# Kernel optimization log

Hardware: AMD Instinct MI355X
Metric: run time of the kernel (lower is better)

## Reference

```python
import jax, jax.numpy as jnp
import numpy as np

EPS = 1e-08
ATOM_CA = 1


def setup_inputs() -> dict:
    key = jax.random.key(0)
    k1, k2 = jax.random.split(key)
    B, N_RES, N_ATOMS = 256, 1024, 37
    pred_coords = jax.random.normal(k1, (B, N_RES, N_ATOMS, 3), dtype=jnp.float32)
    true_coords = jax.random.normal(k2, (B, N_RES, N_ATOMS, 3), dtype=jnp.float32)
    atom_mask = jnp.ones((B, N_RES, N_ATOMS), dtype=jnp.float32)
    return {"pred_coords": pred_coords, "true_coords": true_coords, "atom_mask": atom_mask}


def _kabsch_align(pred, true, mask):
    # pred/true: [B, N, 3], mask: [B, N]
    mask_sum = jnp.sum(mask, axis=1, keepdims=True) + EPS          # [B, 1]
    m = mask[..., None]                                             # [B, N, 1]
    pred_center = jnp.sum(pred * m, axis=1) / mask_sum              # [B, 3]
    true_center = jnp.sum(true * m, axis=1) / mask_sum              # [B, 3]
    pred_c = (pred - pred_center[:, None, :]) * m                   # [B, N, 3]
    true_c = (true - true_center[:, None, :]) * m                   # [B, N, 3]
    H = jnp.einsum('bni,bnj->bij', pred_c, true_c)                  # [B, 3, 3]
    U, s, Vh = jnp.linalg.svd(H)                                    # H = U diag(s) Vh
    V = jnp.swapaxes(Vh, -1, -2)
    Ut = jnp.swapaxes(U, -1, -2)
    det = jnp.linalg.det(jnp.matmul(V, Ut))                         # [B]
    sign = jnp.stack([jnp.ones_like(det), jnp.ones_like(det), det], axis=-1)  # [B, 3]
    S = jnp.eye(3, dtype=pred.dtype) * sign[:, None, :]             # diag(1,1,det)
    R = jnp.matmul(jnp.matmul(V, S), Ut)                            # [B, 3, 3]
    # aligned = (pred - pred_center) @ R^T + true_center
    aligned = jnp.einsum('bnj,bij->bni', pred - pred_center[:, None, :], R)
    return aligned + true_center[:, None, :]


def reference(pred_coords, true_coords, atom_mask):
    pred_ca = pred_coords[:, :, ATOM_CA, :]   # [B, N_res, 3]
    true_ca = true_coords[:, :, ATOM_CA, :]
    ca_mask = atom_mask[:, :, ATOM_CA]        # [B, N_res]
    pred_ca = _kabsch_align(pred_ca, true_ca, ca_mask)
    diff_sq = jnp.sum((pred_ca - true_ca) ** 2, axis=-1)            # [B, N_res]
    rmsd = jnp.sqrt(jnp.sum(diff_sq * ca_mask, axis=1) / (jnp.sum(ca_mask, axis=1) + EPS))
    return jnp.mean(rmsd)
```

## Files before the change

kernel.cpp:

```cpp
#include <hip/hip_runtime.h>
#include <math.h>

#define N_RES 1024
#define N_ATOMS 37
#define ATOM_CA 1
#define NBATCH 256
#define SLICES 2
#define NSUM 18

struct F3 { float x, y, z; };

__global__ __launch_bounds__(256) void rmsd_fused_kernel(
    const float* __restrict__ pred, const float* __restrict__ truec,
    const float* __restrict__ mask, float* __restrict__ partials,
    unsigned int* __restrict__ ticket, float* __restrict__ out)
{
    const int blk   = blockIdx.x;
    const int b     = blk >> 1;
    const int slice = blk & 1;
    const int tid   = threadIdx.x;
    const int n0    = slice * 512 + tid;

    const size_t resStride = (size_t)N_ATOMS * 3;
    const size_t r0 = (size_t)b * N_RES + n0;
    const size_t r1 = r0 + 256;

    const F3 P0 = *reinterpret_cast<const F3*>(pred  + r0 * resStride + ATOM_CA * 3);
    const F3 T0 = *reinterpret_cast<const F3*>(truec + r0 * resStride + ATOM_CA * 3);
    const F3 P1 = *reinterpret_cast<const F3*>(pred  + r1 * resStride + ATOM_CA * 3);
    const F3 T1 = *reinterpret_cast<const F3*>(truec + r1 * resStride + ATOM_CA * 3);
    const float m0 = mask[r0 * N_ATOMS + ATOM_CA];
    const float m1 = mask[r1 * N_ATOMS + ATOM_CA];

    float acc[NSUM];
    acc[0] = m0 + m1;
    acc[1] = m0 * P0.x + m1 * P1.x;
    acc[2] = m0 * P0.y + m1 * P1.y;
    acc[3] = m0 * P0.z + m1 * P1.z;
    acc[4] = m0 * T0.x + m1 * T1.x;
    acc[5] = m0 * T0.y + m1 * T1.y;
    acc[6] = m0 * T0.z + m1 * T1.z;
    acc[7] = m0 * (P0.x*P0.x + P0.y*P0.y + P0.z*P0.z)
           + m1 * (P1.x*P1.x + P1.y*P1.y + P1.z*P1.z);
    acc[8] = m0 * (T0.x*T0.x + T0.y*T0.y + T0.z*T0.z)
           + m1 * (T1.x*T1.x + T1.y*T1.y + T1.z*T1.z);
    acc[9]  = m0 * P0.x * T0.x + m1 * P1.x * T1.x;
    acc[10] = m0 * P0.x * T0.y + m1 * P1.x * T1.y;
    acc[11] = m0 * P0.x * T0.z + m1 * P1.x * T1.z;
    acc[12] = m0 * P0.y * T0.x + m1 * P1.y * T1.x;
    acc[13] = m0 * P0.y * T0.y + m1 * P1.y * T1.y;
    acc[14] = m0 * P0.y * T0.z + m1 * P1.y * T1.z;
    acc[15] = m0 * P0.z * T0.x + m1 * P1.z * T1.x;
    acc[16] = m0 * P0.z * T0.y + m1 * P1.z * T1.y;
    acc[17] = m0 * P0.z * T0.z + m1 * P1.z * T1.z;

#pragma unroll
    for (int i = 0; i < NSUM; ++i) {
        float v = acc[i];
#pragma unroll
        for (int off = 32; off > 0; off >>= 1) v += __shfl_down(v, off, 64);
        acc[i] = v;
    }

    __shared__ float partial[4][NSUM];
    const int wave = tid >> 6, lane = tid & 63;
    if (lane == 0) {
#pragma unroll
        for (int i = 0; i < NSUM; ++i) partial[wave][i] = acc[i];
    }
    __syncthreads();
    if (tid < NSUM) {
        partials[(size_t)blk * NSUM + tid] =
            partial[0][tid] + partial[1][tid] + partial[2][tid] + partial[3][tid];
    }

    __threadfence();
    __syncthreads();
    __shared__ bool amLast;
    if (tid == 0)
        amLast = (atomicAdd(ticket, 1u) == (unsigned)(gridDim.x - 1));
    __syncthreads();
    if (!amLast) return;
    __threadfence();

    {
        const int bb = tid;
        double s[NSUM];
#pragma unroll
        for (int i = 0; i < NSUM; ++i) s[i] = 0.0;
#pragma unroll
        for (int k = 0; k < SLICES; ++k) {
            const float* row = partials + ((size_t)bb * SLICES + k) * NSUM;
#pragma unroll
            for (int i = 0; i < NSUM; ++i) s[i] += (double)row[i];
        }

        const double M   = s[0];
        const double Mep = M + 1e-8;
        const double Sp0 = s[1], Sp1 = s[2], Sp2 = s[3];
        const double St0 = s[4], St1 = s[5], St2 = s[6];
        const double pc0 = Sp0 / Mep, pc1 = Sp1 / Mep, pc2 = Sp2 / Mep;
        const double tc0 = St0 / Mep, tc1 = St1 / Mep, tc2 = St2 / Mep;
        const double Qp = s[7], Qt = s[8];

        const double Sxx = s[9]  - pc0 * St0 - tc0 * Sp0 + pc0 * tc0 * M;
        const double Sxy = s[10] - pc0 * St1 - tc1 * Sp0 + pc0 * tc1 * M;
        const double Sxz = s[11] - pc0 * St2 - tc2 * Sp0 + pc0 * tc2 * M;
        const double Syx = s[12] - pc1 * St0 - tc0 * Sp1 + pc1 * tc0 * M;
        const double Syy = s[13] - pc1 * St1 - tc1 * Sp1 + pc1 * tc1 * M;
        const double Syz = s[14] - pc1 * St2 - tc2 * Sp1 + pc1 * tc2 * M;
        const double Szx = s[15] - pc2 * St0 - tc0 * Sp2 + pc2 * tc0 * M;
        const double Szy = s[16] - pc2 * St1 - tc1 * Sp2 + pc2 * tc1 * M;
        const double Szz = s[17] - pc2 * St2 - tc2 * Sp2 + pc2 * tc2 * M;

        const double Qpc = Qp - 2.0*(pc0*Sp0 + pc1*Sp1 + pc2*Sp2)
                         + (pc0*pc0 + pc1*pc1 + pc2*pc2) * M;
        const double Qtc = Qt - 2.0*(tc0*St0 + tc1*St1 + tc2*St2)
                         + (tc0*tc0 + tc1*tc1 + tc2*tc2) * M;

        const double Sxx2 = Sxx*Sxx, Syy2 = Syy*Syy, Szz2 = Szz*Szz;
        const double Sxy2 = Sxy*Sxy, Syz2 = Syz*Syz, Sxz2 = Sxz*Sxz;
        const double Syx2 = Syx*Syx, Szy2 = Szy*Szy, Szx2 = Szx*Szx;

        const double SyzSzymSyySzz2 = 2.0*(Syz*Szy - Syy*Szz);
        const double Sxx2Syy2Szz2Syz2Szy2 = Syy2 + Szz2 - Sxx2 + Syz2 + Szy2;

        const double C2 = -2.0*(Sxx2 + Syy2 + Szz2 + Sxy2 + Syx2 + Sxz2 + Szx2 + Syz2 + Szy2);
        const double C1 = 8.0*(Sxx*Syz*Szy + Syy*Szx*Sxz + Szz*Sxy*Syx
                             - Sxx*Syy*Szz - Syz*Szx*Sxy - Szy*Syx*Sxz);

        const double SxzpSzx = Sxz + Szx;
        const double SyzpSzy = Syz + Szy;
        const double SxypSyx = Sxy + Syx;
        const double SyzmSzy = Syz - Szy;
        const double SxzmSzx = Sxz - Szx;
        const double SxymSyx = Sxy - Syx;
        const double SxxpSyy = Sxx + Syy;
        const double SxxmSyy = Sxx - Syy;
        const double Sxy2Sxz2Syx2Szx2 = Sxy2 + Sxz2 - Syx2 - Szx2;

        const double C0 =
            Sxy2Sxz2Syx2Szx2 * Sxy2Sxz2Syx2Szx2
          + (Sxx2Syy2Szz2Syz2Szy2 + SyzSzymSyySzz2) * (Sxx2Syy2Szz2Syz2Szy2 - SyzSzymSyySzz2)
          + (-(SxzpSzx)*(SyzmSzy) + (SxymSyx)*(SxxmSyy - Szz)) *
            (-(SxzmSzx)*(SyzpSzy) + (SxymSyx)*(SxxmSyy + Szz))
          + (-(SxzpSzx)*(SyzpSzy) - (SxypSyx)*(SxxpSyy - Szz)) *
            (-(SxzmSzx)*(SyzmSzy) - (SxypSyx)*(SxxpSyy + Szz))
          + ( (SxypSyx)*(SyzpSzy) + (SxzpSzx)*(SxxmSyy + Szz)) *
            (-(SxymSyx)*(SyzmSzy) + (SxzpSzx)*(SxxpSyy + Szz))
          + ( (SxypSyx)*(SyzmSzy) + (SxzmSzx)*(SxxmSyy - Szz)) *
            (-(SxymSyx)*(SyzpSzy) + (SxzmSzx)*(SxxpSyy - Szz));

        double lam = 0.5 * (Qpc + Qtc);
#pragma unroll
        for (int it = 0; it < 16; ++it) {
            const double x2 = lam * lam;
            const double bq = (x2 + C2) * lam;
            const double aq = bq + C1;
            const double den = 2.0 * x2 * lam + bq + aq;
            const double num = aq * lam + C0;
            const double d = (fabs(den) > 1e-300) ? (num / den) : 0.0;
            lam -= d;
        }

        double D = Qpc + Qtc - 2.0 * lam;
        if (D < 0.0) D = 0.0;
        float rmsd = (float)sqrt(D / Mep);

#pragma unroll
        for (int off = 32; off > 0; off >>= 1) rmsd += __shfl_down(rmsd, off, 64);
        __shared__ float part[4];
        if ((tid & 63) == 0) part[tid >> 6] = rmsd;
        __syncthreads();
        if (tid == 0)
            out[0] = (part[0] + part[1] + part[2] + part[3]) * (1.0f / (float)NBATCH);
    }
}

extern "C" void kernel_launch(void* const* d_in, const int* in_sizes, int n_in,
                              void* d_out, int out_size, void* d_ws, size_t ws_size,
                              hipStream_t stream) {
    const float* pred  = (const float*)d_in[0];
    const float* truec = (const float*)d_in[1];
    const float* mask  = (const float*)d_in[2];
    float* out = (float*)d_out;
    float* partials = (float*)d_ws;
    unsigned int* ticket = (unsigned int*)((char*)d_ws + 512 * NSUM * sizeof(float));

    hipMemsetAsync(ticket, 0, sizeof(unsigned int), stream);
    rmsd_fused_kernel<<<NBATCH * SLICES, 256, 0, stream>>>(
        pred, truec, mask, partials, ticket, out);
}
```

Before: 282.4 us.

## Stage full residue coordinate chunks in shared memory via coalesced float4 loads

Each block now handles 256 residues and copies the full per-residue atom coordinates and masks into LDS with contiguous float4 loads. Each wave then picks its CA atom from shared memory. The grid doubles to four slices per batch. This swaps strided gathers for coalesced streaming but reads every atom rather than just the CA, which greatly increases bytes moved and adds many block-wide barriers.

```diff
diff --git a/kernel.cpp b/kernel.cpp
--- a/kernel.cpp
+++ b/kernel.cpp
@@ -5,68 +5,85 @@
 #define N_ATOMS 37
 #define ATOM_CA 1
 #define NBATCH 256
-#define SLICES 2
+#define BLOCKS 1024
+#define SLICES 4
 #define NSUM 18
 
-struct F3 { float x, y, z; };
+#define CQ_F4 1776
+#define MQ_F4 592
 
 __global__ __launch_bounds__(256) void rmsd_fused_kernel(
     const float* __restrict__ pred, const float* __restrict__ truec,
     const float* __restrict__ mask, float* __restrict__ partials,
     unsigned int* __restrict__ ticket, float* __restrict__ out)
 {
-    const int blk   = blockIdx.x;
-    const int b     = blk >> 1;
-    const int slice = blk & 1;
-    const int tid   = threadIdx.x;
-    const int n0    = slice * 512 + tid;
-
-    const size_t resStride = (size_t)N_ATOMS * 3;
-    const size_t r0 = (size_t)b * N_RES + n0;
-    const size_t r1 = r0 + 256;
-
-    const F3 P0 = *reinterpret_cast<const F3*>(pred  + r0 * resStride + ATOM_CA * 3);
-    const F3 T0 = *reinterpret_cast<const F3*>(truec + r0 * resStride + ATOM_CA * 3);
-    const F3 P1 = *reinterpret_cast<const F3*>(pred  + r1 * resStride + ATOM_CA * 3);
-    const F3 T1 = *reinterpret_cast<const F3*>(truec + r1 * resStride + ATOM_CA * 3);
-    const float m0 = mask[r0 * N_ATOMS + ATOM_CA];
-    const float m1 = mask[r1 * N_ATOMS + ATOM_CA];
+    const int blk = blockIdx.x;
+    const int b   = blk >> 2;
+    const int s   = blk & 3;
+    const int tid = threadIdx.x;
+    const int wq  = tid >> 6;
+    const int i   = tid & 63;
+
+    __shared__ __align__(16) float cbuf[CQ_F4 * 4];
+    __shared__ __align__(16) float mbuf[MQ_F4 * 4];
+
+    const size_t resBase = (size_t)b * N_RES + (size_t)s * 256;
+    const int    eb = i * 111 + 3;
+    const int    mb = i * 37 + ATOM_CA;
+
+    float m = 0.f, p0 = 0.f, p1 = 0.f, p2 = 0.f, t0 = 0.f, t1 = 0.f, t2 = 0.f;
+
+#pragma unroll
+    for (int q = 0; q < 4; ++q) {
+        const float4* pq = reinterpret_cast<const float4*>(pred + (resBase + 64u*q) * 111);
+        const float4* mq = reinterpret_cast<const float4*>(mask + (resBase + 64u*q) * 37);
+        float4* c4 = reinterpret_cast<float4*>(cbuf);
+        float4* m4 = reinterpret_cast<float4*>(mbuf);
+        __syncthreads();
+        for (int idx = tid; idx < CQ_F4 + MQ_F4; idx += 256) {
+            if (idx < CQ_F4) c4[idx] = pq[idx];
+            else             m4[idx - CQ_F4] = mq[idx - CQ_F4];
+        }
+        __syncthreads();
+        if (wq == q) {
+            p0 = cbuf[eb]; p1 = cbuf[eb + 1]; p2 = cbuf[eb + 2];
+            m  = mbuf[mb];
+        }
+    }
+#pragma unroll
+    for (int q = 0; q < 4; ++q) {
+        const float4* tq = reinterpret_cast<const float4*>(truec + (resBase + 64u*q) * 111);
+        float4* c4 = reinterpret_cast<float4*>(cbuf);
+        __syncthreads();
+        for (int idx = tid; idx < CQ_F4; idx += 256) c4[idx] = tq[idx];
+        __syncthreads();
+        if (wq == q) {
+            t0 = cbuf[eb]; t1 = cbuf[eb + 1]; t2 = cbuf[eb + 2];
+        }
+    }
 
     float acc[NSUM];
-    acc[0] = m0 + m1;
-    acc[1] = m0 * P0.x + m1 * P1.x;
-    acc[2] = m0 * P0.y + m1 * P1.y;
-    acc[3] = m0 * P0.z + m1 * P1.z;
-    acc[4] = m0 * T0.x + m1 * T1.x;
-    acc[5] = m0 * T0.y + m1 * T1.y;
-    acc[6] = m0 * T0.z + m1 * T1.z;
-    acc[7] = m0 * (P0.x*P0.x + P0.y*P0.y + P0.z*P0.z)
-           + m1 * (P1.x*P1.x + P1.y*P1.y + P1.z*P1.z);
-    acc[8] = m0 * (T0.x*T0.x + T0.y*T0.y + T0.z*T0.z)
-           + m1 * (T1.x*T1.x + T1.y*T1.y + T1.z*T1.z);
-    acc[9]  = m0 * P0.x * T0.x + m1 * P1.x * T1.x;
-    acc[10] = m0 * P0.x * T0.y + m1 * P1.x * T1.y;
-    acc[11] = m0 * P0.x * T0.z + m1 * P1.x * T1.z;
-    acc[12] = m0 * P0.y * T0.x + m1 * P1.y * T1.x;
-    acc[13] = m0 * P0.y * T0.y + m1 * P1.y * T1.y;
-    acc[14] = m0 * P0.y * T0.z + m1 * P1.y * T1.z;
-    acc[15] = m0 * P0.z * T0.x + m1 * P1.z * T1.x;
-    acc[16] = m0 * P0.z * T0.y + m1 * P1.z * T1.y;
-    acc[17] = m0 * P0.z * T0.z + m1 * P1.z * T1.z;
-
-#pragma unroll
-    for (int i = 0; i < NSUM; ++i) {
-        float v = acc[i];
+    acc[0] = m;
+    acc[1] = m * p0;  acc[2] = m * p1;  acc[3] = m * p2;
+    acc[4] = m * t0;  acc[5] = m * t1;  acc[6] = m * t2;
+    acc[7] = m * (p0*p0 + p1*p1 + p2*p2);
+    acc[8] = m * (t0*t0 + t1*t1 + t2*t2);
+    acc[9]  = m * p0 * t0; acc[10] = m * p0 * t1; acc[11] = m * p0 * t2;
+    acc[12] = m * p1 * t0; acc[13] = m * p1 * t1; acc[14] = m * p1 * t2;
+    acc[15] = m * p2 * t0; acc[16] = m * p2 * t1; acc[17] = m * p2 * t2;
+
+#pragma unroll
+    for (int k = 0; k < NSUM; ++k) {
+        float v = acc[k];
 #pragma unroll
         for (int off = 32; off > 0; off >>= 1) v += __shfl_down(v, off, 64);
-        acc[i] = v;
+        acc[k] = v;
     }
 
     __shared__ float partial[4][NSUM];
-    const int wave = tid >> 6, lane = tid & 63;
-    if (lane == 0) {
-#pragma unroll
-        for (int i = 0; i < NSUM; ++i) partial[wave][i] = acc[i];
+    if (i == 0) {
+#pragma unroll
+        for (int k = 0; k < NSUM; ++k) partial[wq][k] = acc[k];
     }
     __syncthreads();
     if (tid < NSUM) {
@@ -85,33 +102,33 @@
 
     {
         const int bb = tid;
-        double s[NSUM];
-#pragma unroll
-        for (int i = 0; i < NSUM; ++i) s[i] = 0.0;
+        double sm[NSUM];
+#pragma unroll
+        for (int k = 0; k < NSUM; ++k) sm[k] = 0.0;
 #pragma unroll
         for (int k = 0; k < SLICES; ++k) {
             const float* row = partials + ((size_t)bb * SLICES + k) * NSUM;
 #pragma unroll
-            for (int i = 0; i < NSUM; ++i) s[i] += (double)row[i];
-        }
-
-        const double M   = s[0];
+            for (int j = 0; j < NSUM; ++j) sm[j] += (double)row[j];
+        }
+
+        const double M   = sm[0];
         const double Mep = M + 1e-8;
-        const double Sp0 = s[1], Sp1 = s[2], Sp2 = s[3];
-        const double St0 = s[4], St1 = s[5], St2 = s[6];
+        const double Sp0 = sm[1], Sp1 = sm[2], Sp2 = sm[3];
+        const double St0 = sm[4], St1 = sm[5], St2 = sm[6];
         const double pc0 = Sp0 / Mep, pc1 = Sp1 / Mep, pc2 = Sp2 / Mep;
         const double tc0 = St0 / Mep, tc1 = St1 / Mep, tc2 = St2 / Mep;
-        const double Qp = s[7], Qt = s[8];
-
-        const double Sxx = s[9]  - pc0 * St0 - tc0 * Sp0 + pc0 * tc0 * M;
-        const double Sxy = s[10] - pc0 * St1 - tc1 * Sp0 + pc0 * tc1 * M;
-        const double Sxz = s[11] - pc0 * St2 - tc2 * Sp0 + pc0 * tc2 * M;
-        const double Syx = s[12] - pc1 * St0 - tc0 * Sp1 + pc1 * tc0 * M;
-        const double Syy = s[13] - pc1 * St1 - tc1 * Sp1 + pc1 * tc1 * M;
-        const double Syz = s[14] - pc1 * St2 - tc2 * Sp1 + pc1 * tc2 * M;
-        const double Szx = s[15] - pc2 * St0 - tc0 * Sp2 + pc2 * tc0 * M;
-        const double Szy = s[16] - pc2 * St1 - tc1 * Sp2 + pc2 * tc1 * M;
-        const double Szz = s[17] - pc2 * St2 - tc2 * Sp2 + pc2 * tc2 * M;
+        const double Qp = sm[7], Qt = sm[8];
+
+        const double Sxx = sm[9]  - pc0 * St0 - tc0 * Sp0 + pc0 * tc0 * M;
+        const double Sxy = sm[10] - pc0 * St1 - tc1 * Sp0 + pc0 * tc1 * M;
+        const double Sxz = sm[11] - pc0 * St2 - tc2 * Sp0 + pc0 * tc2 * M;
+        const double Syx = sm[12] - pc1 * St0 - tc0 * Sp1 + pc1 * tc0 * M;
+        const double Syy = sm[13] - pc1 * St1 - tc1 * Sp1 + pc1 * tc1 * M;
+        const double Syz = sm[14] - pc1 * St2 - tc2 * Sp1 + pc1 * tc2 * M;
+        const double Szx = sm[15] - pc2 * St0 - tc0 * Sp2 + pc2 * tc0 * M;
+        const double Szy = sm[16] - pc2 * St1 - tc1 * Sp2 + pc2 * tc1 * M;
+        const double Szz = sm[17] - pc2 * St2 - tc2 * Sp2 + pc2 * tc2 * M;
 
         const double Qpc = Qp - 2.0*(pc0*Sp0 + pc1*Sp1 + pc2*Sp2)
                          + (pc0*pc0 + pc1*pc1 + pc2*pc2) * M;
@@ -185,9 +202,9 @@
     const float* mask  = (const float*)d_in[2];
     float* out = (float*)d_out;
     float* partials = (float*)d_ws;
-    unsigned int* ticket = (unsigned int*)((char*)d_ws + 512 * NSUM * sizeof(float));
+    unsigned int* ticket = (unsigned int*)((char*)d_ws + BLOCKS * NSUM * sizeof(float));
 
     hipMemsetAsync(ticket, 0, sizeof(unsigned int), stream);
-    rmsd_fused_kernel<<<NBATCH * SLICES, 256, 0, stream>>>(
+    rmsd_fused_kernel<<<BLOCKS, 256, 0, stream>>>(
         pred, truec, mask, partials, ticket, out);
 }
```

Measured after the change: 364.4 us. +29.0%, slower.
